# Kernel optimization log

Measured on AMD Instinct MI355X. Metric: run time of the kernel, lower is better.

## Reference

```python
import jax, jax.numpy as jnp
import numpy as np


def mha(x, mask, wq, bq, wk, bk, wv, bv, wo, bo, n_heads):
    # Flaubert/XLM MultiHeadAttention (eval mode, dropout = identity).
    bs, qlen, dim = x.shape
    dph = dim // n_heads

    def split_heads(t):  # (bs, qlen, dim) -> (bs, n_heads, qlen, dph)
        return t.reshape(bs, qlen, n_heads, dph).transpose(0, 2, 1, 3)

    q = split_heads(x @ wq + bq) / jnp.sqrt(jnp.asarray(dph, x.dtype))
    k = split_heads(x @ wk + bk)
    v = split_heads(x @ wv + bv)

    scores = jnp.einsum('bhqd,bhkd->bhqk', q, k)  # (bs, h, qlen, klen)
    neg = jnp.finfo(scores.dtype).min
    scores = jnp.where((mask == 0)[:, None, None, :], neg, scores)
    weights = jax.nn.softmax(scores, axis=-1)
    ctx = jnp.einsum('bhqk,bhkd->bhqd', weights, v)
    ctx = ctx.transpose(0, 2, 1, 3).reshape(bs, qlen, dim)
    return ctx @ wo + bo


def setup_inputs() -> dict:
    key = jax.random.key(0)
    ks = jax.random.split(key, 20)
    bs, slen = 4, 1024
    d0, d1 = 192, 66
    std = 0.02
    inp = {
        'x': jax.random.normal(ks[0], (bs, slen, d0), jnp.float32),
        'y': jax.random.normal(ks[1], (bs, slen, d1), jnp.float32),
        'mask0': jax.random.randint(ks[2], (bs, slen), 0, 2, jnp.int32),
        'mask1': jax.random.randint(ks[3], (bs, slen), 0, 2, jnp.int32),
    }
    names0 = ['q0', 'k0', 'v0', 'o0']
    names1 = ['q1', 'k1', 'v1', 'o1']
    for i, n in enumerate(names0):
        inp[n + '_w'] = jax.random.normal(ks[4 + i], (d0, d0), jnp.float32) * std
        inp[n + '_b'] = jnp.zeros((d0,), jnp.float32)
    for i, n in enumerate(names1):
        inp[n + '_w'] = jax.random.normal(ks[8 + i], (d1, d1), jnp.float32) * std
        inp[n + '_b'] = jnp.zeros((d1,), jnp.float32)
    return inp


def reference(x, y, mask0, mask1,
              q0_w, q0_b, k0_w, k0_b, v0_w, v0_b, o0_w, o0_b,
              q1_w, q1_b, k1_w, k1_b, v1_w, v1_b, o1_w, o1_b):
    out0 = mha(x, mask0, q0_w, q0_b, k0_w, k0_b, v0_w, v0_b, o0_w, o0_b, n_heads=16)
    out1 = mha(y, mask1, q1_w, q1_b, k1_w, k1_b, v1_w, v1_b, o1_w, o1_b, n_heads=11)
    return (out0, out1)
```

## Files before the change

### kernel.cpp

```cpp
#include <hip/hip_runtime.h>
#include <math.h>


#define BS 4
#define SLEN 1024

#define Q0_OFF 0
#define C0_OFF 786432
#define Q1_OFF 1572864
#define C1_OFF 1843200
#define K0H_OFF 2113536
#define V0T_OFF 2506752
#define K1H_OFF 2899968
#define V1T_OFF 3080192

#define OUT0_SIZE 786432

typedef _Float16 f16x2 __attribute__((ext_vector_type(2)));
typedef _Float16 f16x4 __attribute__((ext_vector_type(4)));
typedef _Float16 f16x8 __attribute__((ext_vector_type(8)));
typedef float f32x4 __attribute__((ext_vector_type(4)));

union F16x8U { f16x8 v8; f16x4 v4[2]; };

__device__ __forceinline__ void mfma_chunk(const _Float16* sA, const _Float16* sWT,
                                           int wv, int lane, f32x4 acc[4])
{
  const int col = lane & 15, grp = lane >> 4;
#pragma unroll
  for (int ks = 0; ks < 2; ++ks) {
    const f16x8 bf = *(const f16x8*)(sWT + (wv * 16 + col) * 72 + ks * 32 + grp * 8);
#pragma unroll
    for (int mt = 0; mt < 4; ++mt) {
      const f16x8 af = *(const f16x8*)(sA + (mt * 16 + col) * 72 + ks * 32 + grp * 8);
      acc[mt] = __builtin_amdgcn_mfma_f32_16x16x32_f16(af, bf, acc[mt], 0, 0, 0);
    }
  }
}

__device__ __forceinline__ void mfma_chunk_split(
    const _Float16* sAh, const _Float16* sAl,
    const _Float16* sWTh, const _Float16* sWTl,
    int wv, int lane, f32x4 acc[4])
{
  const int col = lane & 15, grp = lane >> 4;
#pragma unroll
  for (int ks = 0; ks < 2; ++ks) {
    const int boff = (wv * 16 + col) * 72 + ks * 32 + grp * 8;
    const f16x8 bh = *(const f16x8*)(sWTh + boff);
    const f16x8 bl = *(const f16x8*)(sWTl + boff);
#pragma unroll
    for (int mt = 0; mt < 4; ++mt) {
      const int aoff = (mt * 16 + col) * 72 + ks * 32 + grp * 8;
      const f16x8 ah = *(const f16x8*)(sAh + aoff);
      const f16x8 al = *(const f16x8*)(sAl + aoff);
      acc[mt] = __builtin_amdgcn_mfma_f32_16x16x32_f16(ah, bh, acc[mt], 0, 0, 0);
      acc[mt] = __builtin_amdgcn_mfma_f32_16x16x32_f16(ah, bl, acc[mt], 0, 0, 0);
      acc[mt] = __builtin_amdgcn_mfma_f32_16x16x32_f16(al, bh, acc[mt], 0, 0, 0);
    }
  }
}

template <int DIM>
__device__ __forceinline__ void stage_chunk(const float* __restrict__ A, int row0,
                                            int kc, const float* __restrict__ W,
                                            int col0, _Float16* sA, _Float16* sWT,
                                            int tid)
{
  for (int idx = tid; idx < 2048; idx += 256) {
    const int m = idx >> 5, k = (idx & 31) * 2;
    float2 v = make_float2(0.f, 0.f);
    if (kc + k < DIM) v = *(const float2*)(A + (size_t)(row0 + m) * DIM + kc + k);
    *(f16x2*)(sA + m * 72 + k) = (f16x2){(_Float16)v.x, (_Float16)v.y};
  }
  for (int idx = tid; idx < 2048; idx += 256) {
    const int k = idx >> 5, n = (idx & 31) * 2;
    float2 v = make_float2(0.f, 0.f);
    if (kc + k < DIM && col0 + n < DIM)
      v = *(const float2*)(W + (size_t)(kc + k) * DIM + col0 + n);
    sWT[n * 72 + k] = (_Float16)v.x;
    sWT[(n + 1) * 72 + k] = (_Float16)v.y;
  }
}

template <int DIM>
__device__ __forceinline__ void stage_chunk_split(
    const float* __restrict__ A, int row0, int kc,
    const float* __restrict__ W, int col0,
    _Float16* sAh, _Float16* sAl, _Float16* sWTh, _Float16* sWTl, int tid)
{
  for (int idx = tid; idx < 2048; idx += 256) {
    const int m = idx >> 5, k = (idx & 31) * 2;
    float2 v = make_float2(0.f, 0.f);
    if (kc + k < DIM) v = *(const float2*)(A + (size_t)(row0 + m) * DIM + kc + k);
    const _Float16 hx = (_Float16)v.x, hy = (_Float16)v.y;
    *(f16x2*)(sAh + m * 72 + k) = (f16x2){hx, hy};
    *(f16x2*)(sAl + m * 72 + k) =
        (f16x2){(_Float16)(v.x - (float)hx), (_Float16)(v.y - (float)hy)};
  }
  for (int idx = tid; idx < 2048; idx += 256) {
    const int k = idx >> 5, n = (idx & 31) * 2;
    float2 v = make_float2(0.f, 0.f);
    if (kc + k < DIM && col0 + n < DIM)
      v = *(const float2*)(W + (size_t)(kc + k) * DIM + col0 + n);
    const _Float16 hx = (_Float16)v.x, hy = (_Float16)v.y;
    sWTh[n * 72 + k] = hx;
    sWTh[(n + 1) * 72 + k] = hy;
    sWTl[n * 72 + k] = (_Float16)(v.x - (float)hx);
    sWTl[(n + 1) * 72 + k] = (_Float16)(v.y - (float)hy);
  }
}

template <int DIM, int H, int DPH, int NT, int NCH, int KST>
__device__ void qkv_impl(int bid, const float* __restrict__ X,
                         const float* __restrict__ qw, const float* __restrict__ qb,
                         const float* __restrict__ kw, const float* __restrict__ kb,
                         const float* __restrict__ vw, const float* __restrict__ vb,
                         float* __restrict__ qo, _Float16* __restrict__ kh,
                         _Float16* __restrict__ vth, char* smem)
{
  const int mt64 = bid & 63;
  const int rest = bid >> 6;
  const int mat = rest / NT;
  const int nt = rest % NT;
  const int row0 = mt64 * 64, col0 = nt * 64;

  const float* W = (mat == 0) ? qw : (mat == 1) ? kw : vw;
  const float* B = (mat == 0) ? qb : (mat == 1) ? kb : vb;
  const float scale = (mat == 0) ? (1.0f / sqrtf((float)DPH)) : 1.0f;

  _Float16* sA = (_Float16*)smem;
  _Float16* sWT = sA + 64 * 72;

  const int tid = threadIdx.x;
  const int wv = tid >> 6, lane = tid & 63;
  f32x4 acc[4] = {{0.f,0.f,0.f,0.f},{0.f,0.f,0.f,0.f},{0.f,0.f,0.f,0.f},{0.f,0.f,0.f,0.f}};

  for (int c = 0; c < NCH; ++c) {
    __syncthreads();
    stage_chunk<DIM>(X, row0, c * 64, W, col0, sA, sWT, tid);
    __syncthreads();
    mfma_chunk(sA, sWT, wv, lane, acc);
  }

  const int col = lane & 15, grp = lane >> 4;
  const int cidx = col0 + wv * 16 + col;
  if (cidx < DIM) {
    const float bias = B[cidx];
    const int h = cidx / DPH, d = cidx % DPH;
#pragma unroll
    for (int mt = 0; mt < 4; ++mt) {
#pragma unroll
      for (int r = 0; r < 4; ++r) {
        const int m = row0 + mt * 16 + grp * 4 + r;
        const int b = m >> 10, s = m & 1023;
        const float v = acc[mt][r] + bias;
        const int bh = b * H + h;
        if (mat == 0)
          qo[(size_t)((bh << 10) + s) * DPH + d] = v * scale;
        else if (mat == 1)
          kh[(size_t)((bh << 10) + s) * KST + d] = (_Float16)v;
        else
          vth[((size_t)(bh * DPH + d) << 10) + s] = (_Float16)v;
      }
    }
  }
}

__global__ __launch_bounds__(256) void qkv_kernel(
    const float* __restrict__ x, const float* __restrict__ y,
    const float* __restrict__ q0w, const float* __restrict__ q0b,
    const float* __restrict__ k0w, const float* __restrict__ k0b,
    const float* __restrict__ v0w, const float* __restrict__ v0b,
    const float* __restrict__ q1w, const float* __restrict__ q1b,
    const float* __restrict__ k1w, const float* __restrict__ k1b,
    const float* __restrict__ v1w, const float* __restrict__ v1b,
    float* __restrict__ ws)
{
  extern __shared__ char smem[];
  _Float16* hws = (_Float16*)ws;
  const int bid = blockIdx.x;
  if (bid < 576)
    qkv_impl<192, 16, 12, 3, 3, 12>(bid, x, q0w, q0b, k0w, k0b, v0w, v0b,
                                    ws + Q0_OFF, hws + 2 * (size_t)K0H_OFF,
                                    hws + 2 * (size_t)V0T_OFF, smem);
  else
    qkv_impl<66, 11, 6, 2, 2, 8>(bid - 576, y, q1w, q1b, k1w, k1b, v1w, v1b,
                                 ws + Q1_OFF, hws + 2 * (size_t)K1H_OFF,
                                 hws + 2 * (size_t)V1T_OFF, smem);
}

template <int H, int DPH, int SKP>
__device__ void attn_impl(int bid, const float* __restrict__ qg,
                          const _Float16* __restrict__ kh,
                          const _Float16* __restrict__ vth,
                          const int* __restrict__ mask,
                          float* __restrict__ ctx, char* smem)
{
  constexpr int CH = 128;
  constexpr int NCH = SLEN / CH;
  constexpr int KBUF = CH * SKP + 32;
  constexpr int VST = 136;

  _Float16* sK = (_Float16*)smem;
  _Float16* sVT = sK + 2 * KBUF;
  float* sB = (float*)(sVT + 2 * DPH * VST);
  _Float16* sP = (_Float16*)(sB + 2 * CH);

  const int bh = bid >> 4;
  const int b = bh / H;
  const int h = bh % H;
  const int tid = threadIdx.x;

  const float* qb_ = qg + (size_t)bh * SLEN * DPH;
  const _Float16* kb_ = kh + (size_t)bh * SLEN * SKP;
  const _Float16* vb_ = vth + ((size_t)bh * DPH << 10);
  const int* mb_ = mask + b * SLEN;

  if (tid < 64) sK[(tid >> 5) * KBUF + CH * SKP + (tid & 31)] = (_Float16)0.f;

  const int wave = tid >> 6, lane = tid & 63;
  const int col = lane & 15, grp = lane >> 4;
  const int qtile = (bid & 15) * 4 + wave;

  f16x8 aq;
  {
    const int qrow = qtile * 16 + col;
#pragma unroll
    for (int j = 0; j < 8; ++j) {
      const int d = grp * 8 + j;
      aq[j] = (d < DPH) ? (_Float16)qb_[(size_t)qrow * DPH + d] : (_Float16)0.f;
    }
  }

  auto stage = [&](int cc, int pb) {
    const uint4* srcK = (const uint4*)(kb_ + (size_t)cc * CH * SKP);
    uint4* dstK = (uint4*)(sK + pb * KBUF);
    for (int idx = tid; idx < CH * SKP / 8; idx += 256) dstK[idx] = srcK[idx];
    _Float16* dV = sVT + pb * DPH * VST;
    for (int idx = tid; idx < DPH * 16; idx += 256) {
      const int d = idx >> 4, q = idx & 15;
      *(uint4*)(dV + d * VST + q * 8) =
          ((const uint4*)(vb_ + ((size_t)d << 10) + cc * CH))[q];
    }
    float* dB = sB + pb * CH;
    for (int idx = tid; idx < CH; idx += 256)
      dB[idx] = mb_[cc * CH + idx] ? 0.f : -64.f;
  };

  stage(0, 0);
  __syncthreads();

  f32x4 Oacc[2] = {{0.f,0.f,0.f,0.f},{0.f,0.f,0.f,0.f}};
  float lsum[4] = {0.f,0.f,0.f,0.f};

#pragma unroll 1
  for (int c = 0; c < NCH; ++c) {
    const int p = c & 1;
    if (c + 1 < NCH) stage(c + 1, p ^ 1);

    const _Float16* sKp = sK + p * KBUF;
    const _Float16* sVp = sVT + p * DPH * VST;
    const float* sBp = sB + p * CH;
    const int de = (col < DPH) ? col : 0;

#pragma unroll
    for (int kc = 0; kc < CH / 32; ++kc) {
#pragma unroll
      for (int t = 0; t < 2; ++t) {
        const int kt = kc * 2 + t;
        F16x8U kf;
        {
          const _Float16* kp = sKp + (kt * 16 + col) * SKP + grp * 8;
          kf.v4[0] = *(const f16x4*)kp;
          kf.v4[1] = *(const f16x4*)(kp + 4);
        }
        const float bb = sBp[kt * 16 + col];
        const f32x4 biasv = {bb, bb, bb, bb};
        f32x4 S = __builtin_amdgcn_mfma_f32_16x16x32_f16(aq, kf.v8, biasv,
                                                         0, 0, 0);
        _Float16* pw = sP + wave * 640 + t * 16 + col;
#pragma unroll
        for (int r = 0; r < 4; ++r) {
          const float e = __expf(S[r]);
          lsum[r] += e;
          pw[(grp * 4 + r) * 40] = (_Float16)e;
        }
      }
      const f16x8 vf = *(const f16x8*)(sVp + de * VST + kc * 32 + grp * 8);
      const f16x8 pf = *(const f16x8*)(sP + wave * 640 + col * 40 + grp * 8);
      Oacc[kc & 1] =
          __builtin_amdgcn_mfma_f32_16x16x32_f16(pf, vf, Oacc[kc & 1], 0, 0, 0);
    }
    __syncthreads();
  }

#pragma unroll
  for (int r = 0; r < 4; ++r) {
    float v = lsum[r];
    v += __shfl_xor(v, 1);
    v += __shfl_xor(v, 2);
    v += __shfl_xor(v, 4);
    v += __shfl_xor(v, 8);
    lsum[r] = v;
  }
  if (col < DPH) {
    const int qrow0 = qtile * 16;
#pragma unroll
    for (int r = 0; r < 4; ++r) {
      const int row = qrow0 + grp * 4 + r;
      const float o = (Oacc[0][r] + Oacc[1][r]) / lsum[r];
      ctx[(size_t)(b * SLEN + row) * (H * DPH) + h * DPH + col] = o;
    }
  }
}

__global__ __launch_bounds__(256) void attn_kernel(
    const int* __restrict__ mask0, const int* __restrict__ mask1,
    float* __restrict__ ws)
{
  extern __shared__ char smem[];
  _Float16* hws = (_Float16*)ws;
  const int bid = blockIdx.x;
  if (bid < 1024)
    attn_impl<16, 12, 12>(bid, ws + Q0_OFF, hws + 2 * (size_t)K0H_OFF,
                          hws + 2 * (size_t)V0T_OFF, mask0, ws + C0_OFF, smem);
  else
    attn_impl<11, 6, 8>(bid - 1024, ws + Q1_OFF, hws + 2 * (size_t)K1H_OFF,
                        hws + 2 * (size_t)V1T_OFF, mask1, ws + C1_OFF, smem);
}

template <int DIM, int NCH>
__device__ void oproj_impl(int bid, const float* __restrict__ Cx,
                           const float* __restrict__ ow, const float* __restrict__ ob,
                           float* __restrict__ out, char* smem)
{
  const int mt64 = bid & 63;
  const int nt = bid >> 6;
  const int row0 = mt64 * 64, col0 = nt * 64;

  _Float16* sAh = (_Float16*)smem;
  _Float16* sAl = sAh + 64 * 72;
  _Float16* sWTh = sAl + 64 * 72;
  _Float16* sWTl = sWTh + 64 * 72;

  const int tid = threadIdx.x;
  const int wv = tid >> 6, lane = tid & 63;
  f32x4 acc[4] = {{0.f,0.f,0.f,0.f},{0.f,0.f,0.f,0.f},{0.f,0.f,0.f,0.f},{0.f,0.f,0.f,0.f}};

  for (int c = 0; c < NCH; ++c) {
    __syncthreads();
    stage_chunk_split<DIM>(Cx, row0, c * 64, ow, col0, sAh, sAl, sWTh, sWTl, tid);
    __syncthreads();
    mfma_chunk_split(sAh, sAl, sWTh, sWTl, wv, lane, acc);
  }

  const int col = lane & 15, grp = lane >> 4;
  const int cidx = col0 + wv * 16 + col;
  if (cidx < DIM) {
    const float bias = ob[cidx];
#pragma unroll
    for (int mt = 0; mt < 4; ++mt) {
#pragma unroll
      for (int r = 0; r < 4; ++r) {
        const int m = row0 + mt * 16 + grp * 4 + r;
        out[(size_t)m * DIM + cidx] = acc[mt][r] + bias;
      }
    }
  }
}

__global__ __launch_bounds__(256) void oproj_kernel(
    const float* __restrict__ o0w, const float* __restrict__ o0b,
    const float* __restrict__ o1w, const float* __restrict__ o1b,
    float* __restrict__ ws, float* __restrict__ out)
{
  extern __shared__ char smem[];
  const int bid = blockIdx.x;
  if (bid < 192)
    oproj_impl<192, 3>(bid, ws + C0_OFF, o0w, o0b, out, smem);
  else
    oproj_impl<66, 2>(bid - 192, ws + C1_OFF, o1w, o1b, out + OUT0_SIZE, smem);
}

extern "C" void kernel_launch(void* const* d_in, const int* in_sizes, int n_in,
                              void* d_out, int out_size, void* d_ws, size_t ws_size,
                              hipStream_t stream)
{
  const float* x = (const float*)d_in[0];
  const float* y = (const float*)d_in[1];
  const int* mask0 = (const int*)d_in[2];
  const int* mask1 = (const int*)d_in[3];
  const float* q0w = (const float*)d_in[4];  const float* q0b = (const float*)d_in[5];
  const float* k0w = (const float*)d_in[6];  const float* k0b = (const float*)d_in[7];
  const float* v0w = (const float*)d_in[8];  const float* v0b = (const float*)d_in[9];
  const float* o0w = (const float*)d_in[10]; const float* o0b = (const float*)d_in[11];
  const float* q1w = (const float*)d_in[12]; const float* q1b = (const float*)d_in[13];
  const float* k1w = (const float*)d_in[14]; const float* k1b = (const float*)d_in[15];
  const float* v1w = (const float*)d_in[16]; const float* v1b = (const float*)d_in[17];
  const float* o1w = (const float*)d_in[18]; const float* o1b = (const float*)d_in[19];

  float* ws = (float*)d_ws;
  float* out = (float*)d_out;

  const int qkv_smem = 2 * 64 * 72 * 2;
  const int oproj_smem = 4 * 64 * 72 * 2;
  const int attn_smem = 2 * (128 * 12 + 32) * 2 + 2 * 12 * 136 * 2
                      + 2 * 128 * 4 + 4 * 640 * 2;

  qkv_kernel<<<960, 256, qkv_smem, stream>>>(x, y, q0w, q0b, k0w, k0b, v0w, v0b,
                                             q1w, q1b, k1w, k1b, v1w, v1b, ws);
  attn_kernel<<<1728, 256, attn_smem, stream>>>(mask0, mask1, ws);
  oproj_kernel<<<320, 256, oproj_smem, stream>>>(o0w, o0b, o1w, o1b, ws, out);
}
```

Measured before the change: 171.4 us.

## Compute softmax row sums via ones column in V MFMA, pad P stride

Adds a row of ones to the transposed V tile so the P·V MFMA produces the softmax denominator in an otherwise unused output column, removing per-element lsum accumulation and the shuffle reduction. The two score MFMAs per 32-key chunk are issued back to back, and the P scratch stride changes from 40 to 44 to alter LDS bank mapping. The cost is a little more shared memory and a denominator accumulated from fp16-rounded probabilities rather than fp32 exponentials.

New measurement: 168.0 us. No clear change (-1.9%).

```diff
diff --git a/kernel.cpp b/kernel.cpp
--- a/kernel.cpp
+++ b/kernel.cpp
@@ -201,10 +201,13 @@
   constexpr int NCH = SLEN / CH;
   constexpr int KBUF = CH * SKP + 32;
   constexpr int VST = 136;
+  constexpr int VROWS = DPH + 1;
+  constexpr int PST = 44;
+  constexpr int PWAVE = 16 * PST;
 
   _Float16* sK = (_Float16*)smem;
   _Float16* sVT = sK + 2 * KBUF;
-  float* sB = (float*)(sVT + 2 * DPH * VST);
+  float* sB = (float*)(sVT + 2 * VROWS * VST);
   _Float16* sP = (_Float16*)(sB + 2 * CH);
 
   const int bh = bid >> 4;
@@ -218,6 +221,10 @@
   const int* mb_ = mask + b * SLEN;
 
   if (tid < 64) sK[(tid >> 5) * KBUF + CH * SKP + (tid & 31)] = (_Float16)0.f;
+  for (int idx = tid; idx < 2 * CH; idx += 256) {
+    const int pb = idx / CH, q = idx % CH;
+    sVT[(pb * VROWS + DPH) * VST + q] = (_Float16)1.f;
+  }
 
   const int wave = tid >> 6, lane = tid & 63;
   const int col = lane & 15, grp = lane >> 4;
@@ -237,7 +244,7 @@
     const uint4* srcK = (const uint4*)(kb_ + (size_t)cc * CH * SKP);
     uint4* dstK = (uint4*)(sK + pb * KBUF);
     for (int idx = tid; idx < CH * SKP / 8; idx += 256) dstK[idx] = srcK[idx];
-    _Float16* dV = sVT + pb * DPH * VST;
+    _Float16* dV = sVT + pb * VROWS * VST;
     for (int idx = tid; idx < DPH * 16; idx += 256) {
       const int d = idx >> 4, q = idx & 15;
       *(uint4*)(dV + d * VST + q * 8) =
@@ -252,7 +259,7 @@
   __syncthreads();
 
   f32x4 Oacc[2] = {{0.f,0.f,0.f,0.f},{0.f,0.f,0.f,0.f}};
-  float lsum[4] = {0.f,0.f,0.f,0.f};
+  const int de = (col <= DPH) ? col : 0;
 
 #pragma unroll 1
   for (int c = 0; c < NCH; ++c) {
@@ -260,57 +267,59 @@
     if (c + 1 < NCH) stage(c + 1, p ^ 1);
 
     const _Float16* sKp = sK + p * KBUF;
-    const _Float16* sVp = sVT + p * DPH * VST;
+    const _Float16* sVp = sVT + p * VROWS * VST;
     const float* sBp = sB + p * CH;
-    const int de = (col < DPH) ? col : 0;
 
 #pragma unroll
     for (int kc = 0; kc < CH / 32; ++kc) {
-#pragma unroll
-      for (int t = 0; t < 2; ++t) {
-        const int kt = kc * 2 + t;
-        F16x8U kf;
-        {
-          const _Float16* kp = sKp + (kt * 16 + col) * SKP + grp * 8;
-          kf.v4[0] = *(const f16x4*)kp;
-          kf.v4[1] = *(const f16x4*)(kp + 4);
-        }
-        const float bb = sBp[kt * 16 + col];
-        const f32x4 biasv = {bb, bb, bb, bb};
-        f32x4 S = __builtin_amdgcn_mfma_f32_16x16x32_f16(aq, kf.v8, biasv,
-                                                         0, 0, 0);
-        _Float16* pw = sP + wave * 640 + t * 16 + col;
-#pragma unroll
-        for (int r = 0; r < 4; ++r) {
-          const float e = __expf(S[r]);
-          lsum[r] += e;
-          pw[(grp * 4 + r) * 40] = (_Float16)e;
-        }
+      F16x8U kf0, kf1;
+      {
+        const _Float16* kp0 = sKp + ((kc * 2) * 16 + col) * SKP + grp * 8;
+        const _Float16* kp1 = sKp + ((kc * 2 + 1) * 16 + col) * SKP + grp * 8;
+        kf0.v4[0] = *(const f16x4*)kp0;
+        kf0.v4[1] = *(const f16x4*)(kp0 + 4);
+        kf1.v4[0] = *(const f16x4*)kp1;
+        kf1.v4[1] = *(const f16x4*)(kp1 + 4);
       }
+      const float bb0 = sBp[kc * 32 + col];
+      const float bb1 = sBp[kc * 32 + 16 + col];
+      const f32x4 S0 = __builtin_amdgcn_mfma_f32_16x16x32_f16(
+          aq, kf0.v8, (f32x4){bb0, bb0, bb0, bb0}, 0, 0, 0);
+      const f32x4 S1 = __builtin_amdgcn_mfma_f32_16x16x32_f16(
+          aq, kf1.v8, (f32x4){bb1, bb1, bb1, bb1}, 0, 0, 0);
+
+      _Float16* pw = sP + wave * PWAVE + col;
+#pragma unroll
+      for (int r = 0; r < 4; ++r) {
+        pw[(grp * 4 + r) * PST] = (_Float16)__expf(S0[r]);
+        pw[(grp * 4 + r) * PST + 16] = (_Float16)__expf(S1[r]);
+      }
+
       const f16x8 vf = *(const f16x8*)(sVp + de * VST + kc * 32 + grp * 8);
-      const f16x8 pf = *(const f16x8*)(sP + wave * 640 + col * 40 + grp * 8);
+      F16x8U pf;
+      {
+        const _Float16* pr = sP + wave * PWAVE + col * PST + grp * 8;
+        pf.v4[0] = *(const f16x4*)pr;
+        pf.v4[1] = *(const f16x4*)(pr + 4);
+      }
       Oacc[kc & 1] =
-          __builtin_amdgcn_mfma_f32_16x16x32_f16(pf, vf, Oacc[kc & 1], 0, 0, 0);
+          __builtin_amdgcn_mfma_f32_16x16x32_f16(pf.v8, vf, Oacc[kc & 1], 0, 0, 0);
     }
     __syncthreads();
   }
 
-#pragma unroll
-  for (int r = 0; r < 4; ++r) {
-    float v = lsum[r];
-    v += __shfl_xor(v, 1);
-    v += __shfl_xor(v, 2);
-    v += __shfl_xor(v, 4);
-    v += __shfl_xor(v, 8);
-    lsum[r] = v;
-  }
+  f32x4 Osum;
+#pragma unroll
+  for (int r = 0; r < 4; ++r) Osum[r] = Oacc[0][r] + Oacc[1][r];
+  float lq[4];
+#pragma unroll
+  for (int r = 0; r < 4; ++r) lq[r] = __shfl(Osum[r], (lane & 48) + DPH);
   if (col < DPH) {
     const int qrow0 = qtile * 16;
 #pragma unroll
     for (int r = 0; r < 4; ++r) {
       const int row = qrow0 + grp * 4 + r;
-      const float o = (Oacc[0][r] + Oacc[1][r]) / lsum[r];
-      ctx[(size_t)(b * SLEN + row) * (H * DPH) + h * DPH + col] = o;
+      ctx[(size_t)(b * SLEN + row) * (H * DPH) + h * DPH + col] = Osum[r] / lq[r];
     }
   }
 }
@@ -405,8 +414,8 @@
 
   const int qkv_smem = 2 * 64 * 72 * 2;
   const int oproj_smem = 4 * 64 * 72 * 2;
-  const int attn_smem = 2 * (128 * 12 + 32) * 2 + 2 * 12 * 136 * 2
-                      + 2 * 128 * 4 + 4 * 640 * 2;
+  const int attn_smem = 2 * (128 * 12 + 32) * 2 + 2 * 13 * 136 * 2
+                      + 2 * 128 * 4 + 4 * (16 * 44) * 2;
 
   qkv_kernel<<<960, 256, qkv_smem, stream>>>(x, y, q0w, q0b, k0w, k0b, v0w, v0b,
                                              q1w, q1b, k1w, k1b, v1w, v1b, ws);
```
